# Kernel optimization log

Measured on AMD Instinct MI355X. Metric: run time of the kernel, lower is better.

The kernel has to match this reference:

```python
import jax, jax.numpy as jnp
import numpy as np

N_NODES = 50000
N_EDGES = 800000
IN_FEATS = 64
OUT_FEATS = 64
EDGE_DIM = 8


def setup_inputs() -> dict:
    key = jax.random.key(0)
    k1, k2, k3, k4, k5 = jax.random.split(key, 5)
    node_feat = jax.random.normal(k1, (N_NODES, IN_FEATS), dtype=jnp.float32)
    edge_feat = jax.random.normal(k2, (N_EDGES, EDGE_DIM), dtype=jnp.float32)
    W = jax.random.normal(k3, (OUT_FEATS, IN_FEATS), dtype=jnp.float32) * (1.0 / np.sqrt(IN_FEATS))
    b = jnp.zeros((OUT_FEATS,), dtype=jnp.float32)
    src = jax.random.randint(k4, (N_EDGES,), 0, N_NODES, dtype=jnp.int64 if jax.config.jax_enable_x64 else jnp.int32)
    dst = jax.random.randint(k5, (N_EDGES,), 0, N_NODES, dtype=jnp.int64 if jax.config.jax_enable_x64 else jnp.int32)
    return {"node_feat": node_feat, "edge_feat": edge_feat, "W": W, "b": b,
            "src": src, "dst": dst}


def reference(node_feat, edge_feat, W, b, src, dst):
    # EfConv forward with aggregate='sum', node_feat.shape[1] == in_feats.
    n_nodes = node_feat.shape[0]
    edge_dim = edge_feat.shape[1]
    h_src = node_feat[src]  # [E, in_feats] gather once, reused for every slice
    aggs = []
    for k in range(edge_dim):  # small fixed loop over edge feature slices
        m = h_src * edge_feat[:, k:k + 1]                      # u_mul_e: [E, in_feats]
        aggs.append(jax.ops.segment_sum(m, dst, num_segments=n_nodes))
    agg = jnp.stack(aggs, axis=1)                              # [N, edge_dim, in_feats]
    # per-slice shared linear, then concat along feature dim
    out = jnp.einsum('nki,oi->nko', agg, W) + b                # [N, edge_dim, out_feats]
    return out.reshape(n_nodes, edge_dim * W.shape[0])         # [N, edge_dim*out_feats]
```

## Files before the change

### kernel.cpp

```cpp
#include <hip/hip_runtime.h>


#define FEATS 64
#define EDGE_DIM 8

typedef _Float16 half8 __attribute__((ext_vector_type(8)));
typedef float f32x4 __attribute__((ext_vector_type(4)));

__global__ void __launch_bounds__(256) fused_kernel(
    const int* __restrict__ dst, int* __restrict__ deg, int* __restrict__ rank,
    int n_edges, int nbH, int nbC,
    const float* __restrict__ ef, half8* __restrict__ efh,
    const float* __restrict__ nf, const float* __restrict__ W,
    _Float16* __restrict__ t, int n_nodes)
{
    const int tid = threadIdx.x;
    const unsigned bid = blockIdx.x;

    if (bid < (unsigned)nbH) {
        long i8 = ((long)bid * 256 + tid) * 8;
        if (i8 + 7 < n_edges) {
            int4 d0 = *(const int4*)(dst + i8);
            int4 d1 = *(const int4*)(dst + i8 + 4);
            int4 r0, r1;
            r0.x = atomicAdd(&deg[d0.x], 1);
            r0.y = atomicAdd(&deg[d0.y], 1);
            r0.z = atomicAdd(&deg[d0.z], 1);
            r0.w = atomicAdd(&deg[d0.w], 1);
            r1.x = atomicAdd(&deg[d1.x], 1);
            r1.y = atomicAdd(&deg[d1.y], 1);
            r1.z = atomicAdd(&deg[d1.z], 1);
            r1.w = atomicAdd(&deg[d1.w], 1);
            *(int4*)(rank + i8)     = r0;
            *(int4*)(rank + i8 + 4) = r1;
        } else {
            for (long e = i8; e < n_edges; ++e)
                rank[e] = atomicAdd(&deg[dst[e]], 1);
        }
        return;
    }

    if (bid < (unsigned)(nbH + nbC)) {
        int e = (bid - nbH) * 256 + tid;
        if (e < n_edges) {
            const f32x4* q = (const f32x4*)(ef + (long)e * EDGE_DIM);
            f32x4 a = q[0], c = q[1];
            half8 h;
            h[0] = (_Float16)a.x; h[1] = (_Float16)a.y;
            h[2] = (_Float16)a.z; h[3] = (_Float16)a.w;
            h[4] = (_Float16)c.x; h[5] = (_Float16)c.y;
            h[6] = (_Float16)c.z; h[7] = (_Float16)c.w;
            efh[e] = h;
        }
        return;
    }

    __shared__ float sWt[FEATS * 65];
    __shared__ float srow[4][FEATS];
    const int bt = bid - nbH - nbC;

    #pragma unroll
    for (int base = 0; base < FEATS * FEATS; base += 256) {
        int idx = base + tid;
        int o = idx >> 6;
        int i = idx & 63;
        sWt[i * 65 + o] = W[idx];
    }

    const int r = tid >> 6;
    const int o = tid & 63;
    const int node = bt * 4 + r;
    if (node < n_nodes) srow[r][o] = nf[(long)node * FEATS + o];
    __syncthreads();

    if (node >= n_nodes) return;
    float sum = 0.f;
    #pragma unroll
    for (int i = 0; i < FEATS; i++)
        sum += srow[r][i] * sWt[i * 65 + o];
    t[(long)node * FEATS + o] = (_Float16)sum;
}

__global__ void __launch_bounds__(256) partials_kernel(
    const int* __restrict__ deg, int* __restrict__ partials, int n)
{
    __shared__ int s[256];
    int i = blockIdx.x * 256 + threadIdx.x;
    s[threadIdx.x] = (i < n) ? deg[i] : 0;
    __syncthreads();
    for (int off = 128; off > 0; off >>= 1) {
        if (threadIdx.x < off) s[threadIdx.x] += s[threadIdx.x + off];
        __syncthreads();
    }
    if (threadIdx.x == 0) partials[blockIdx.x] = s[0];
}

__global__ void __launch_bounds__(256) scan_addback_kernel(
    const int* __restrict__ deg, const int* __restrict__ partials,
    int* __restrict__ offsets, int nb, int n, int n_edges)
{
    __shared__ int sp[256];
    __shared__ int s[256];
    const int tid = threadIdx.x;

    sp[tid] = (tid < nb) ? partials[tid] : 0;
    for (int off = 1; off < 256; off <<= 1) {
        __syncthreads();
        int x = (tid >= off) ? sp[tid - off] : 0;
        __syncthreads();
        sp[tid] += x;
    }

    int i = blockIdx.x * 256 + tid;
    int v = (i < n) ? deg[i] : 0;
    s[tid] = v;
    for (int off = 1; off < 256; off <<= 1) {
        __syncthreads();
        int x = (tid >= off) ? s[tid - off] : 0;
        __syncthreads();
        s[tid] += x;
    }
    __syncthreads();

    if (i < n) {
        int pbase = (blockIdx.x == 0) ? 0 : sp[blockIdx.x - 1];
        offsets[i] = pbase + s[tid] - v;
    }
    if (blockIdx.x == 0 && tid == 0) offsets[n] = n_edges;
}

__global__ void __launch_bounds__(256) permute_ef_kernel(
    const int* __restrict__ src, const int* __restrict__ dst,
    const int* __restrict__ rank, const int* __restrict__ offsets,
    const half8* __restrict__ efh,
    int* __restrict__ srcs, half8* __restrict__ efs, int n_edges)
{
    int i4 = (blockIdx.x * 256 + threadIdx.x) * 4;
    if (i4 + 3 < n_edges) {
        int4 s = *(const int4*)(src + i4);
        int4 d = *(const int4*)(dst + i4);
        int4 r = *(const int4*)(rank + i4);
        int p0 = offsets[d.x] + r.x;
        int p1 = offsets[d.y] + r.y;
        int p2 = offsets[d.z] + r.z;
        int p3 = offsets[d.w] + r.w;
        half8 h0 = efh[i4], h1 = efh[i4 + 1], h2 = efh[i4 + 2], h3 = efh[i4 + 3];
        efs[p0] = h0;
        efs[p1] = h1;
        efs[p2] = h2;
        efs[p3] = h3;
        srcs[p0] = s.x; srcs[p1] = s.y; srcs[p2] = s.z; srcs[p3] = s.w;
    } else {
        for (int e = i4; e < n_edges; ++e) {
            int p = offsets[dst[e]] + rank[e];
            srcs[p] = src[e];
            efs[p] = efh[e];
        }
    }
}

#define CHUNK 16

__global__ void __launch_bounds__(256) aggregate_seq_kernel(
    const _Float16* __restrict__ t, const half8* __restrict__ efs,
    const int* __restrict__ srcs, const int* __restrict__ offsets,
    const float* __restrict__ b, float* __restrict__ out, int n_nodes)
{
    const int node = __builtin_amdgcn_readfirstlane(
        (int)((blockIdx.x * 256 + threadIdx.x) >> 6));
    const int o = threadIdx.x & 63;
    if (node >= n_nodes) return;

    const int beg = offsets[node];
    const int end = offsets[node + 1];
    float acc[EDGE_DIM];
    #pragma unroll
    for (int k = 0; k < EDGE_DIM; k++) acc[k] = 0.f;

    if (end > beg) {
        const int last = end - 1;
        for (int j = beg; j < end; j += CHUNK) {
            int sidx[CHUNK];
            #pragma unroll
            for (int u = 0; u < CHUNK; u++) {
                int jj = j + u;
                sidx[u] = srcs[jj <= last ? jj : last];
            }
            float tv[CHUNK];
            #pragma unroll
            for (int u = 0; u < CHUNK; u++)
                tv[u] = (float)t[(long)sidx[u] * FEATS + o];
            #pragma unroll
            for (int u = 0; u < CHUNK; u++) {
                int jj = j + u;
                int ej = jj <= last ? jj : last;
                float tvm = (jj <= last) ? tv[u] : 0.f;
                half8 row = efs[ej];
                #pragma unroll
                for (int k = 0; k < EDGE_DIM; k++)
                    acc[k] += (float)row[k] * tvm;
            }
        }
    }

    const float bo = b[o];
    float* op = out + (long)node * (EDGE_DIM * FEATS) + o;
    #pragma unroll
    for (int k = 0; k < EDGE_DIM; k++)
        __builtin_nontemporal_store(acc[k] + bo, op + k * FEATS);
}

extern "C" void kernel_launch(void* const* d_in, const int* in_sizes, int n_in,
                              void* d_out, int out_size, void* d_ws, size_t ws_size,
                              hipStream_t stream) {
    const float* node_feat = (const float*)d_in[0];
    const float* edge_feat = (const float*)d_in[1];
    const float* W         = (const float*)d_in[2];
    const float* b         = (const float*)d_in[3];
    const int*   src       = (const int*)d_in[4];
    const int*   dst       = (const int*)d_in[5];
    float* out = (float*)d_out;

    const int n_nodes = in_sizes[0] / FEATS;
    const int n_edges = in_sizes[4];
    const int nb_nodes = (n_nodes + 255) / 256;
    const int nbH = (n_edges + 2047) / 2048;
    const int nbC = (n_edges + 255) / 256;
    const int nbT = (n_nodes + 3) / 4;
    const int nbP = (n_edges + 1023) / 1024;

    int* w = (int*)d_ws;
    _Float16* t   = (_Float16*)w;
    int* deg      = w + (long)n_nodes * (FEATS / 2);
    int* offsets  = deg + n_nodes;
    int* partials = offsets + n_nodes + 1;
    int* rank     = partials + 256;
    int* srcs     = rank + n_edges;
    uintptr_t ha  = ((uintptr_t)(srcs + n_edges) + 15) & ~(uintptr_t)15;
    half8* efh    = (half8*)ha;
    half8* efs    = efh + n_edges;

    hipMemsetAsync(deg, 0, (size_t)n_nodes * 4, stream);
    fused_kernel<<<nbH + nbC + nbT, 256, 0, stream>>>(
        dst, deg, rank, n_edges, nbH, nbC, edge_feat, efh,
        node_feat, W, t, n_nodes);
    partials_kernel<<<nb_nodes, 256, 0, stream>>>(deg, partials, n_nodes);
    scan_addback_kernel<<<nb_nodes, 256, 0, stream>>>(deg, partials, offsets,
                                                      nb_nodes, n_nodes, n_edges);
    permute_ef_kernel<<<nbP, 256, 0, stream>>>(src, dst, rank, offsets, efh,
                                               srcs, efs, n_edges);

    const long total_ag = (long)n_nodes * 64;
    aggregate_seq_kernel<<<(int)((total_ag + 255) / 256), 256, 0, stream>>>(
        t, efs, srcs, offsets, b, out, n_nodes);
}
```

Before: 271.0 us.

## Privatize degree histogram into 16 planes to reduce atomic contention

The degree-counting atomics are spread across 16 per-block-group copies of the degree array. Each rank value carries its plane tag in its high bits. A merge kernel prefix-sums the planes per node to produce plane offsets and the total degree, and the permute step adds the plane offset when computing each edge's position. The aim is to cut contention on hot degree counters, at the cost of a 16x larger memset, an extra strided read pass in the merge, and one more gather in the permute kernel.

```diff
diff --git a/kernel.cpp b/kernel.cpp
--- a/kernel.cpp
+++ b/kernel.cpp
@@ -3,13 +3,16 @@
 
 #define FEATS 64
 #define EDGE_DIM 8
+#define NPLANE 16
+#define PLANE_SHIFT 26
+#define LOCAL_MASK ((1u << PLANE_SHIFT) - 1u)
 
 typedef _Float16 half8 __attribute__((ext_vector_type(8)));
 typedef float f32x4 __attribute__((ext_vector_type(4)));
 
 __global__ void __launch_bounds__(256) fused_kernel(
-    const int* __restrict__ dst, int* __restrict__ deg, int* __restrict__ rank,
-    int n_edges, int nbH, int nbC,
+    const int* __restrict__ dst, int* __restrict__ deg16,
+    unsigned* __restrict__ rank, int n_edges, int nbH, int nbC,
     const float* __restrict__ ef, half8* __restrict__ efh,
     const float* __restrict__ nf, const float* __restrict__ W,
     _Float16* __restrict__ t, int n_nodes)
@@ -18,24 +21,27 @@
     const unsigned bid = blockIdx.x;
 
     if (bid < (unsigned)nbH) {
+        const unsigned h = bid & (NPLANE - 1);
+        int* __restrict__ degp = deg16 + (long)h * n_nodes;
+        const unsigned htag = h << PLANE_SHIFT;
         long i8 = ((long)bid * 256 + tid) * 8;
         if (i8 + 7 < n_edges) {
             int4 d0 = *(const int4*)(dst + i8);
             int4 d1 = *(const int4*)(dst + i8 + 4);
-            int4 r0, r1;
-            r0.x = atomicAdd(&deg[d0.x], 1);
-            r0.y = atomicAdd(&deg[d0.y], 1);
-            r0.z = atomicAdd(&deg[d0.z], 1);
-            r0.w = atomicAdd(&deg[d0.w], 1);
-            r1.x = atomicAdd(&deg[d1.x], 1);
-            r1.y = atomicAdd(&deg[d1.y], 1);
-            r1.z = atomicAdd(&deg[d1.z], 1);
-            r1.w = atomicAdd(&deg[d1.w], 1);
-            *(int4*)(rank + i8)     = r0;
-            *(int4*)(rank + i8 + 4) = r1;
+            uint4 r0, r1;
+            r0.x = htag | (unsigned)atomicAdd(&degp[d0.x], 1);
+            r0.y = htag | (unsigned)atomicAdd(&degp[d0.y], 1);
+            r0.z = htag | (unsigned)atomicAdd(&degp[d0.z], 1);
+            r0.w = htag | (unsigned)atomicAdd(&degp[d0.w], 1);
+            r1.x = htag | (unsigned)atomicAdd(&degp[d1.x], 1);
+            r1.y = htag | (unsigned)atomicAdd(&degp[d1.y], 1);
+            r1.z = htag | (unsigned)atomicAdd(&degp[d1.z], 1);
+            r1.w = htag | (unsigned)atomicAdd(&degp[d1.w], 1);
+            *(uint4*)(rank + i8)     = r0;
+            *(uint4*)(rank + i8 + 4) = r1;
         } else {
             for (long e = i8; e < n_edges; ++e)
-                rank[e] = atomicAdd(&deg[dst[e]], 1);
+                rank[e] = htag | (unsigned)atomicAdd(&degp[dst[e]], 1);
         }
         return;
     }
@@ -45,12 +51,12 @@
         if (e < n_edges) {
             const f32x4* q = (const f32x4*)(ef + (long)e * EDGE_DIM);
             f32x4 a = q[0], c = q[1];
-            half8 h;
-            h[0] = (_Float16)a.x; h[1] = (_Float16)a.y;
-            h[2] = (_Float16)a.z; h[3] = (_Float16)a.w;
-            h[4] = (_Float16)c.x; h[5] = (_Float16)c.y;
-            h[6] = (_Float16)c.z; h[7] = (_Float16)c.w;
-            efh[e] = h;
+            half8 hh;
+            hh[0] = (_Float16)a.x; hh[1] = (_Float16)a.y;
+            hh[2] = (_Float16)a.z; hh[3] = (_Float16)a.w;
+            hh[4] = (_Float16)c.x; hh[5] = (_Float16)c.y;
+            hh[6] = (_Float16)c.z; hh[7] = (_Float16)c.w;
+            efh[e] = hh;
         }
         return;
     }
@@ -81,18 +87,33 @@
     t[(long)node * FEATS + o] = (_Float16)sum;
 }
 
-__global__ void __launch_bounds__(256) partials_kernel(
-    const int* __restrict__ deg, int* __restrict__ partials, int n)
+__global__ void __launch_bounds__(256) merge_partials_kernel(
+    int* __restrict__ deg16, int* __restrict__ deg,
+    int* __restrict__ partials, int n)
 {
     __shared__ int s[256];
-    int i = blockIdx.x * 256 + threadIdx.x;
-    s[threadIdx.x] = (i < n) ? deg[i] : 0;
+    const int tid = threadIdx.x;
+    int i = blockIdx.x * 256 + tid;
+    int tot = 0;
+    if (i < n) {
+        int run = 0;
+        #pragma unroll
+        for (int x = 0; x < NPLANE; x++) {
+            long idx = (long)x * n + i;
+            int c = deg16[idx];
+            deg16[idx] = run;
+            run += c;
+        }
+        deg[i] = run;
+        tot = run;
+    }
+    s[tid] = tot;
     __syncthreads();
     for (int off = 128; off > 0; off >>= 1) {
-        if (threadIdx.x < off) s[threadIdx.x] += s[threadIdx.x + off];
-        __syncthreads();
-    }
-    if (threadIdx.x == 0) partials[blockIdx.x] = s[0];
+        if (tid < off) s[tid] += s[tid + off];
+        __syncthreads();
+    }
+    if (tid == 0) partials[blockIdx.x] = s[0];
 }
 
 __global__ void __launch_bounds__(256) scan_addback_kernel(
@@ -131,19 +152,23 @@
 
 __global__ void __launch_bounds__(256) permute_ef_kernel(
     const int* __restrict__ src, const int* __restrict__ dst,
-    const int* __restrict__ rank, const int* __restrict__ offsets,
-    const half8* __restrict__ efh,
-    int* __restrict__ srcs, half8* __restrict__ efs, int n_edges)
+    const unsigned* __restrict__ rank, const int* __restrict__ offsets,
+    const int* __restrict__ deg16, const half8* __restrict__ efh,
+    int* __restrict__ srcs, half8* __restrict__ efs, int n_edges, int n_nodes)
 {
     int i4 = (blockIdx.x * 256 + threadIdx.x) * 4;
     if (i4 + 3 < n_edges) {
         int4 s = *(const int4*)(src + i4);
         int4 d = *(const int4*)(dst + i4);
-        int4 r = *(const int4*)(rank + i4);
-        int p0 = offsets[d.x] + r.x;
-        int p1 = offsets[d.y] + r.y;
-        int p2 = offsets[d.z] + r.z;
-        int p3 = offsets[d.w] + r.w;
+        uint4 r = *(const uint4*)(rank + i4);
+        int p0 = offsets[d.x] + deg16[(long)(r.x >> PLANE_SHIFT) * n_nodes + d.x]
+               + (int)(r.x & LOCAL_MASK);
+        int p1 = offsets[d.y] + deg16[(long)(r.y >> PLANE_SHIFT) * n_nodes + d.y]
+               + (int)(r.y & LOCAL_MASK);
+        int p2 = offsets[d.z] + deg16[(long)(r.z >> PLANE_SHIFT) * n_nodes + d.z]
+               + (int)(r.z & LOCAL_MASK);
+        int p3 = offsets[d.w] + deg16[(long)(r.w >> PLANE_SHIFT) * n_nodes + d.w]
+               + (int)(r.w & LOCAL_MASK);
         half8 h0 = efh[i4], h1 = efh[i4 + 1], h2 = efh[i4 + 2], h3 = efh[i4 + 3];
         efs[p0] = h0;
         efs[p1] = h1;
@@ -152,7 +177,10 @@
         srcs[p0] = s.x; srcs[p1] = s.y; srcs[p2] = s.z; srcs[p3] = s.w;
     } else {
         for (int e = i4; e < n_edges; ++e) {
-            int p = offsets[dst[e]] + rank[e];
+            unsigned rr = rank[e];
+            int dd = dst[e];
+            int p = offsets[dd] + deg16[(long)(rr >> PLANE_SHIFT) * n_nodes + dd]
+                  + (int)(rr & LOCAL_MASK);
             srcs[p] = src[e];
             efs[p] = efh[e];
         }
@@ -231,24 +259,25 @@
 
     int* w = (int*)d_ws;
     _Float16* t   = (_Float16*)w;
-    int* deg      = w + (long)n_nodes * (FEATS / 2);
+    int* deg16    = w + (long)n_nodes * (FEATS / 2);
+    int* deg      = deg16 + (long)NPLANE * n_nodes;
     int* offsets  = deg + n_nodes;
     int* partials = offsets + n_nodes + 1;
-    int* rank     = partials + 256;
-    int* srcs     = rank + n_edges;
+    unsigned* rank = (unsigned*)(partials + 256);
+    int* srcs     = (int*)(rank + n_edges);
     uintptr_t ha  = ((uintptr_t)(srcs + n_edges) + 15) & ~(uintptr_t)15;
     half8* efh    = (half8*)ha;
     half8* efs    = efh + n_edges;
 
-    hipMemsetAsync(deg, 0, (size_t)n_nodes * 4, stream);
+    hipMemsetAsync(deg16, 0, (size_t)NPLANE * n_nodes * 4, stream);
     fused_kernel<<<nbH + nbC + nbT, 256, 0, stream>>>(
-        dst, deg, rank, n_edges, nbH, nbC, edge_feat, efh,
+        dst, deg16, rank, n_edges, nbH, nbC, edge_feat, efh,
         node_feat, W, t, n_nodes);
-    partials_kernel<<<nb_nodes, 256, 0, stream>>>(deg, partials, n_nodes);
+    merge_partials_kernel<<<nb_nodes, 256, 0, stream>>>(deg16, deg, partials, n_nodes);
     scan_addback_kernel<<<nb_nodes, 256, 0, stream>>>(deg, partials, offsets,
                                                       nb_nodes, n_nodes, n_edges);
-    permute_ef_kernel<<<nbP, 256, 0, stream>>>(src, dst, rank, offsets, efh,
-                                               srcs, efs, n_edges);
+    permute_ef_kernel<<<nbP, 256, 0, stream>>>(src, dst, rank, offsets, deg16, efh,
+                                               srcs, efs, n_edges, n_nodes);
 
     const long total_ag = (long)n_nodes * 64;
     aggregate_seq_kernel<<<(int)((total_ag + 255) / 256), 256, 0, stream>>>(
```

Result: slower. 277.7 us (+2.5%).
